# Performance work log

Measured on AMD Instinct MI355X. Metric: run time of the kernel, lower is better.

The kernel has to match this reference:

```python
import jax, jax.numpy as jnp
import numpy as np

B_, L_, H_, P_ = 8, 4096, 512, 256
DT_LO, DT_HI = 1e-3, 4e-3  # keep Heinsen log-space weights in fp32 range for L=4096


def setup_inputs() -> dict:
    key = jax.random.key(0)
    ks = jax.random.split(key, 8)
    u = jax.random.normal(ks[0], (B_, L_, H_), dtype=jnp.float32)
    # Diagonal continuous-time state matrix Lambda (HiPPO-N-like: Re=-0.5, structured imag parts)
    lambda_re = -0.5 * jnp.ones((P_,), dtype=jnp.float32)
    lambda_im = jnp.pi * (jnp.arange(P_, dtype=jnp.float32) + 1.0)
    # Input/output projections (complex, stored as re/im pairs)
    B_re = jax.random.normal(ks[1], (P_, H_), dtype=jnp.float32) / jnp.sqrt(float(H_))
    B_im = jax.random.normal(ks[2], (P_, H_), dtype=jnp.float32) / jnp.sqrt(float(H_))
    C_re = jax.random.normal(ks[3], (H_, P_), dtype=jnp.float32) / jnp.sqrt(float(P_))
    C_im = jax.random.normal(ks[4], (H_, P_), dtype=jnp.float32) / jnp.sqrt(float(P_))
    D = jax.random.normal(ks[5], (H_,), dtype=jnp.float32)
    # Per-state learnable log-timescales, log-uniform in [DT_LO, DT_HI]
    log_delta = jax.random.uniform(ks[6], (P_,), dtype=jnp.float32,
                                   minval=jnp.log(DT_LO), maxval=jnp.log(DT_HI))
    return {"u": u, "lambda_re": lambda_re, "lambda_im": lambda_im,
            "B_re": B_re, "B_im": B_im, "C_re": C_re, "C_im": C_im,
            "D": D, "log_delta": log_delta}


def reference(u, lambda_re, lambda_im, B_re, B_im, C_re, C_im, D, log_delta):
    # --- ZOH discretization (eq. 6 of S5 paper) ---
    lam = lambda_re + 1j * lambda_im                     # (P,) complex64
    delta = jnp.exp(log_delta)                           # (P,)
    lambda_bar = jnp.exp(lam * delta)                    # (P,) complex
    B_tilde = B_re + 1j * B_im                           # (P,H)
    B_bar = ((lambda_bar - 1.0) / lam)[:, None] * B_tilde  # (P,H)

    # --- input projection: Bu_k = B_bar @ u_k ---
    Bu = jnp.einsum('blh,ph->blp', u.astype(B_bar.dtype), B_bar)  # (B,L,P) complex

    # --- Heinsen log-space parallel scan: x_k = lambda_bar * x_{k-1} + Bu_k ---
    L = u.shape[1]
    log_lambda = jnp.log(lambda_bar)                     # (P,) complex
    k = jnp.arange(L, dtype=jnp.float32)
    weights = jnp.exp(k[:, None] * log_lambda[None, :])  # (L,P) complex
    xs = weights[None] * jnp.cumsum(Bu / weights[None], axis=1)  # (B,L,P)

    # --- output: y_k = 2*Re(C_tilde x_k) + D*u_k (conjugate symmetry) ---
    C_tilde = C_re + 1j * C_im                           # (H,P)
    y = 2.0 * jnp.real(jnp.einsum('blp,hp->blh', xs, C_tilde)) + D * u
    return y
```

## Files before the change

### kernel.cpp

```cpp
#include <hip/hip_runtime.h>
#include <hip/hip_bf16.h>
#include <math.h>

#define HH 512
#define PP 256
#define LSEQ 4096
#define BB 8
#define MTOT (BB*LSEQ)
#define N2P 512

typedef __attribute__((ext_vector_type(8))) short bf16x8;
typedef __attribute__((ext_vector_type(4))) float f32x4;
typedef __attribute__((ext_vector_type(8))) unsigned short u16x8;
typedef __attribute__((ext_vector_type(4))) unsigned short u16x4;

#define SWZ(row) (((((row) & 7) ^ (((row) >> 3) & 7)) << 4))

__device__ inline unsigned short f2b(float x) {
    return __builtin_bit_cast(unsigned short, __float2bfloat16(x));
}
__device__ inline float b2f(unsigned short h) {
    union { unsigned int u; float f; } v; v.u = ((unsigned int)h) << 16;
    return v.f;
}

#define GLOAD16(gp, lp) __builtin_amdgcn_global_load_lds( \
    (const __attribute__((address_space(1))) unsigned int*)(gp), \
    (__attribute__((address_space(3))) unsigned int*)(lp), 16, 0, 0)

__device__ inline size_t panel_off(int r, int k) {
    int nblk = r >> 7, rl = r & 127;
    int kblk = k >> 6, kl = k & 63;
    int c = kl >> 3, j = kl & 7;
    return (size_t)(nblk * 8 + kblk) * 16384 + rl * 128 + ((c * 16) ^ SWZ(rl)) + j * 2;
}

__global__ void prep_w1_k(const float* __restrict__ lre, const float* __restrict__ lim,
                          const float* __restrict__ logd,
                          const float* __restrict__ Bre, const float* __restrict__ Bim,
                          char* __restrict__ W1s, float2* __restrict__ lamb) {
    int idx = blockIdx.x * 256 + threadIdx.x;
    if (idx >= PP * HH) return;
    int p = idx >> 9;
    int h = idx & (HH - 1);
    float delta = expf(logd[p]);
    float lr = lre[p], li = lim[p];
    float er = expf(lr * delta);
    float th = li * delta;
    float lbr = er * cosf(th), lbi = er * sinf(th);
    if (h == 0) lamb[p] = make_float2(lbr, lbi);
    float a = lbr - 1.0f, b = lbi;
    float n2 = lr * lr + li * li;
    float gr = (a * lr + b * li) / n2;
    float gi = (b * lr - a * li) / n2;
    float br = Bre[idx], bi = Bim[idx];
    *(unsigned short*)(W1s + panel_off(p, h))      = f2b(gr * br - gi * bi);
    *(unsigned short*)(W1s + panel_off(PP + p, h)) = f2b(gr * bi + gi * br);
}

__global__ void prep_w2_k(const float* __restrict__ Cre, const float* __restrict__ Cim,
                          char* __restrict__ W2s) {
    int idx = blockIdx.x * 256 + threadIdx.x;
    if (idx >= HH * N2P) return;
    int h = idx >> 9;
    int k = idx & 511;
    float v = (k < PP) ? 2.0f * Cre[(size_t)h * PP + k]
                       : -2.0f * Cim[(size_t)h * PP + (k - PP)];
    *(unsigned short*)(W2s + panel_off(h, k)) = f2b(v);
}

#define TILE_COMPUTE(ABUF, BBUF) { \
    bf16x8 af[4][2], bfv[2][2]; \
    _Pragma("unroll") for (int f = 0; f < 4; ++f) { \
      int ar = wm + f * 16 + (lane & 15); \
      _Pragma("unroll") for (int kk = 0; kk < 2; ++kk) \
        af[f][kk] = *(const bf16x8*)((ABUF) + ar * 128 + ((kk * 64 + (lane >> 4) * 16) ^ SWZ(ar))); } \
    _Pragma("unroll") for (int g = 0; g < 2; ++g) { \
      int br = wn + g * 16 + (lane & 15); \
      _Pragma("unroll") for (int kk = 0; kk < 2; ++kk) \
        bfv[g][kk] = *(const bf16x8*)((BBUF) + br * 128 + ((kk * 64 + (lane >> 4) * 16) ^ SWZ(br))); } \
    _Pragma("unroll") for (int f = 0; f < 4; ++f) \
      _Pragma("unroll") for (int g = 0; g < 2; ++g) \
        _Pragma("unroll") for (int kk = 0; kk < 2; ++kk) \
          acc[f][g] = __builtin_amdgcn_mfma_f32_16x16x32_bf16(af[f][kk], bfv[g][kk], acc[f][g], 0, 0, 0); }

__global__ __launch_bounds__(512, 4) void gemm1_k(const float* __restrict__ u,
                                                  const char* __restrict__ W1s,
                                                  unsigned short* __restrict__ T1) {
    __shared__ char smem[65536];
    const int tid = threadIdx.x, wave = tid >> 6, lane = tid & 63;
    const int swz = (blockIdx.x & 7) * 128 + (blockIdx.x >> 3);
    const int m0 = (swz >> 2) * 128;
    const int nblk = swz & 3, n0 = nblk * 128;
    const int wm = (wave >> 2) * 64, wn = (wave & 3) * 32;
    const int arow = tid >> 2, acol = tid & 3;

    float4 av0[4], av1[4];
    f32x4 acc[4][2] = {};

#define G1_A_LOAD(SET, K0) { \
    const float* src = &u[(size_t)(m0 + arow) * HH + (K0) + acol * 16]; \
    SET[0] = *(const float4*)src;       SET[1] = *(const float4*)(src + 4); \
    SET[2] = *(const float4*)(src + 8); SET[3] = *(const float4*)(src + 12); }

#define G1_A_WRITE(SET, ABUF) { \
    bf16x8 p0, p1; \
    p0[0] = (short)f2b(SET[0].x); p0[1] = (short)f2b(SET[0].y); \
    p0[2] = (short)f2b(SET[0].z); p0[3] = (short)f2b(SET[0].w); \
    p0[4] = (short)f2b(SET[1].x); p0[5] = (short)f2b(SET[1].y); \
    p0[6] = (short)f2b(SET[1].z); p0[7] = (short)f2b(SET[1].w); \
    p1[0] = (short)f2b(SET[2].x); p1[1] = (short)f2b(SET[2].y); \
    p1[2] = (short)f2b(SET[2].z); p1[3] = (short)f2b(SET[2].w); \
    p1[4] = (short)f2b(SET[3].x); p1[5] = (short)f2b(SET[3].y); \
    p1[6] = (short)f2b(SET[3].z); p1[7] = (short)f2b(SET[3].w); \
    *(bf16x8*)((ABUF) + arow * 128 + ((acol * 32)      ^ SWZ(arow))) = p0; \
    *(bf16x8*)((ABUF) + arow * 128 + ((acol * 32 + 16) ^ SWZ(arow))) = p1; }

#define G1_B_GLOAD(K0, BBUF) { \
    const char* pan = W1s + (size_t)(nblk * 8 + ((K0) >> 6)) * 16384 + tid * 16; \
    GLOAD16(pan, (BBUF) + tid * 16); \
    GLOAD16(pan + 8192, (BBUF) + tid * 16 + 8192); }

    char* A0 = smem;          char* B0 = smem + 16384;
    char* A1 = smem + 32768;  char* B1 = smem + 49152;

    G1_A_LOAD(av1, 0);
    G1_B_GLOAD(0, B0);
    G1_A_LOAD(av0, 64);
    asm volatile("s_waitcnt vmcnt(4)" ::: "memory");
    G1_A_WRITE(av1, A0);
    __syncthreads();

    #pragma unroll
    for (int t = 0; t < 8; ++t) {
        char* Ac = (t & 1) ? A1 : A0; char* Bc = (t & 1) ? B1 : B0;
        char* An = (t & 1) ? A0 : A1; char* Bn = (t & 1) ? B0 : B1;
        if (t < 7) G1_B_GLOAD((t + 1) * 64, Bn);
        if (t < 6) {
            if ((t & 1) == 0) { G1_A_LOAD(av1, (t + 2) * 64); }
            else              { G1_A_LOAD(av0, (t + 2) * 64); }
        }
        TILE_COMPUTE(Ac, Bc);
        if (t < 7) {
            if ((t & 1) == 0) { G1_A_WRITE(av0, An); }
            else              { G1_A_WRITE(av1, An); }
        }
        if (t < 6)       { asm volatile("s_waitcnt vmcnt(4)" ::: "memory"); }
        else if (t == 6) { asm volatile("s_waitcnt vmcnt(0)" ::: "memory"); }
        __syncthreads();
    }

    {
        char* ep = smem;
        #pragma unroll
        for (int f = 0; f < 4; ++f) {
            #pragma unroll
            for (int g = 0; g < 2; ++g) {
                int r = wn + g * 16 + (lane & 15);
                int mb = (wm + f * 16 + ((lane >> 4) << 2)) * 2;
                u16x4 pk;
                pk[0] = f2b(acc[f][g][0]); pk[1] = f2b(acc[f][g][1]);
                pk[2] = f2b(acc[f][g][2]); pk[3] = f2b(acc[f][g][3]);
                *(u16x4*)(ep + r * 256 + (mb ^ ((r & 7) << 4))) = pk;
            }
        }
        __syncthreads();
        #pragma unroll
        for (int it = 0; it < 4; ++it) {
            int r = it * 32 + (tid >> 4);
            int mc = tid & 15;
            u16x8 v = *(const u16x8*)(ep + r * 256 + ((mc * 16) ^ ((r & 7) << 4)));
            *(u16x8*)&T1[(size_t)(n0 + r) * MTOT + m0 + mc * 8] = v;
        }
    }
}

__global__ __launch_bounds__(512, 4) void gemm2_k(const unsigned short* __restrict__ Xs,
                                                  const char* __restrict__ W2s,
                                                  float* __restrict__ y,
                                                  const float* __restrict__ u,
                                                  const float* __restrict__ D) {
    __shared__ char smem[65536];
    const int tid = threadIdx.x, wave = tid >> 6, lane = tid & 63;
    const int swz = (blockIdx.x & 7) * 128 + (blockIdx.x >> 3);
    const int m0 = (swz >> 2) * 128;
    const int nblk = swz & 3, n0 = nblk * 128;
    const int wm = (wave >> 2) * 64, wn = (wave & 3) * 32;
    const int kr = tid >> 5;
    const int mc4 = tid & 31;

    u16x4 xv0[4], xv1[4];
    f32x4 acc[4][2] = {};

#define G2_A_LOAD(SET, K0) { \
    _Pragma("unroll") for (int kk = 0; kk < 4; ++kk) \
        SET[kk] = *(const u16x4*)&Xs[(size_t)((K0) + kr * 4 + kk) * MTOT + m0 + mc4 * 4]; }

#define G2_A_WRITE(SET, ABUF) { \
    _Pragma("unroll") for (int j = 0; j < 4; ++j) { \
        int m = mc4 * 4 + j; \
        u16x4 o; o[0] = SET[0][j]; o[1] = SET[1][j]; o[2] = SET[2][j]; o[3] = SET[3][j]; \
        *(u16x4*)((ABUF) + m * 128 + ((kr * 8) ^ SWZ(m))) = o; } }

#define G2_B_GLOAD(K0, BBUF) { \
    const char* pan = W2s + (size_t)(nblk * 8 + ((K0) >> 6)) * 16384 + tid * 16; \
    GLOAD16(pan, (BBUF) + tid * 16); \
    GLOAD16(pan + 8192, (BBUF) + tid * 16 + 8192); }

    char* A0 = smem;          char* B0 = smem + 16384;
    char* A1 = smem + 32768;  char* B1 = smem + 49152;

    G2_A_LOAD(xv1, 0);
    G2_B_GLOAD(0, B0);
    G2_A_LOAD(xv0, 64);
    asm volatile("s_waitcnt vmcnt(4)" ::: "memory");
    G2_A_WRITE(xv1, A0);
    __syncthreads();

    #pragma unroll
    for (int t = 0; t < 8; ++t) {
        char* Ac = (t & 1) ? A1 : A0; char* Bc = (t & 1) ? B1 : B0;
        char* An = (t & 1) ? A0 : A1; char* Bn = (t & 1) ? B0 : B1;
        if (t < 7) G2_B_GLOAD((t + 1) * 64, Bn);
        if (t < 6) {
            if ((t & 1) == 0) { G2_A_LOAD(xv1, (t + 2) * 64); }
            else              { G2_A_LOAD(xv0, (t + 2) * 64); }
        }
        TILE_COMPUTE(Ac, Bc);
        if (t < 7) {
            if ((t & 1) == 0) { G2_A_WRITE(xv0, An); }
            else              { G2_A_WRITE(xv1, An); }
        }
        if (t < 6)       { asm volatile("s_waitcnt vmcnt(4)" ::: "memory"); }
        else if (t == 6) { asm volatile("s_waitcnt vmcnt(0)" ::: "memory"); }
        __syncthreads();
    }

    float* epi = (float*)smem;
    float* myepi = epi + wave * 2048;
    #pragma unroll
    for (int f = 0; f < 4; ++f) {
        #pragma unroll
        for (int g = 0; g < 2; ++g) {
            int ml = f * 16 + ((lane >> 4) << 2);
            int hl = g * 16 + (lane & 15);
            #pragma unroll
            for (int i = 0; i < 4; ++i)
                myepi[(ml + i) * 32 + hl] = acc[f][g][i];
        }
    }
    __syncthreads();

    #pragma unroll
    for (int it = 0; it < 8; ++it) {
        int idx = it * 512 + tid;
        int ml = idx >> 5, c = idx & 31;
        int w = ((ml >> 6) << 2) + (c >> 3);
        const float4 v = *(const float4*)(epi + w * 2048 + (ml & 63) * 32 + (c & 7) * 4);
        int grow = m0 + ml, gcol = n0 + c * 4;
        const float4 uv = *(const float4*)&u[(size_t)grow * HH + gcol];
        const float4 dv = *(const float4*)&D[gcol];
        float4 o = make_float4(v.x + dv.x * uv.x, v.y + dv.y * uv.y,
                               v.z + dv.z * uv.z, v.w + dv.w * uv.w);
        *(float4*)&y[(size_t)grow * HH + gcol] = o;
    }
}

__global__ __launch_bounds__(256) void scan_k(const unsigned short* __restrict__ T1,
                                              unsigned short* __restrict__ Xs,
                                              const float2* __restrict__ lamb) {
    const int b = blockIdx.x >> 8;
    const int p = blockIdx.x & 255;
    const int t = threadIdx.x;
    const float2 L = lamb[p];

    const size_t baseRe = (size_t)p * MTOT + (size_t)b * LSEQ + t * 16;
    const size_t baseIm = (size_t)(PP + p) * MTOT + (size_t)b * LSEQ + t * 16;

    u16x8 r0 = *(const u16x8*)&T1[baseRe];
    u16x8 r1 = *(const u16x8*)&T1[baseRe + 8];
    u16x8 i0 = *(const u16x8*)&T1[baseIm];
    u16x8 i1 = *(const u16x8*)&T1[baseIm + 8];

    float re[16], im[16];
    #pragma unroll
    for (int j = 0; j < 8; ++j) {
        re[j] = b2f(r0[j]); re[8 + j] = b2f(r1[j]);
        im[j] = b2f(i0[j]); im[8 + j] = b2f(i1[j]);
    }

    float sr = 0.f, si = 0.f;
    #pragma unroll
    for (int j = 0; j < 16; ++j) {
        float nsr = L.x * sr - L.y * si + re[j];
        si = L.x * si + L.y * sr + im[j];
        sr = nsr;
    }

    __shared__ float cr[256], ci[256];
    cr[t] = sr; ci[t] = si;
    __syncthreads();

    float wr = L.x, wi = L.y;
    #pragma unroll
    for (int q = 0; q < 4; ++q) { float nr = wr * wr - wi * wi; wi = 2.f * wr * wi; wr = nr; }

    for (int off = 1; off < 256; off <<= 1) {
        float pr = 0.f, pi = 0.f;
        const bool has = (t >= off);
        if (has) { pr = cr[t - off]; pi = ci[t - off]; }
        __syncthreads();
        if (has) {
            sr += wr * pr - wi * pi;
            si += wr * pi + wi * pr;
            cr[t] = sr; ci[t] = si;
        }
        __syncthreads();
        float nr = wr * wr - wi * wi; wi = 2.f * wr * wi; wr = nr;
    }

    float xr = 0.f, xi = 0.f;
    if (t > 0) { xr = cr[t - 1]; xi = ci[t - 1]; }

    u16x8 o0, o1, o2, o3;
    #pragma unroll
    for (int j = 0; j < 16; ++j) {
        float nr = L.x * xr - L.y * xi + re[j];
        xi = L.x * xi + L.y * xr + im[j];
        xr = nr;
        if (j < 8) { o0[j] = f2b(xr); o2[j] = f2b(xi); }
        else       { o1[j - 8] = f2b(xr); o3[j - 8] = f2b(xi); }
    }
    *(u16x8*)&Xs[baseRe]     = o0;
    *(u16x8*)&Xs[baseRe + 8] = o1;
    *(u16x8*)&Xs[baseIm]     = o2;
    *(u16x8*)&Xs[baseIm + 8] = o3;
}


extern "C" void kernel_launch(void* const* d_in, const int* in_sizes, int n_in,
                              void* d_out, int out_size, void* d_ws, size_t ws_size,
                              hipStream_t stream) {
    const float* u    = (const float*)d_in[0];
    const float* lre  = (const float*)d_in[1];
    const float* lim  = (const float*)d_in[2];
    const float* Bre  = (const float*)d_in[3];
    const float* Bim  = (const float*)d_in[4];
    const float* Cre  = (const float*)d_in[5];
    const float* Cim  = (const float*)d_in[6];
    const float* Dv   = (const float*)d_in[7];
    const float* logd = (const float*)d_in[8];
    float* out = (float*)d_out;

    char* ws = (char*)d_ws;
    char*           W1s  = ws;
    char*           W2s  = ws + (512 << 10);
    float2*         lamb = (float2*)(ws + (1 << 20));
    unsigned short* Xs   = (unsigned short*)(ws + (1 << 20) + 4096);

    unsigned short* T1 = (unsigned short*)d_out;

    prep_w1_k<<<(PP * HH) / 256, 256, 0, stream>>>(lre, lim, logd, Bre, Bim, W1s, lamb);
    prep_w2_k<<<(HH * N2P) / 256, 256, 0, stream>>>(Cre, Cim, W2s);

    gemm1_k<<<1024, 512, 0, stream>>>(u, W1s, T1);
    scan_k<<<BB * PP, 256, 0, stream>>>(T1, Xs, lamb);
    gemm2_k<<<1024, 512, 0, stream>>>(Xs, W2s, out, u, Dv);
}
```

Measured before the change: 97.48 us.

## Pre-convert u to swizzled bf16 panels and load GEMM1 A tiles via direct global-to-LDS copies

Adds a separate kernel that converts the fp32 input u into bf16 tiles laid out in the same swizzled panel format as the weights. GEMM1 then fetches A tiles with the same direct global-to-LDS 16-byte loads it already uses for B, instead of loading fp32 into registers, converting and writing to LDS. This removes the register staging and conversion from GEMM1 and makes the two operand pipelines uniform. The cost is an extra kernel launch and an extra pass over u: a 64 MB fp32 read plus a 32 MB bf16 write and re-read. The main loop also gains a second barrier per iteration.

```diff
diff --git a/kernel.cpp b/kernel.cpp
--- a/kernel.cpp
+++ b/kernel.cpp
@@ -69,6 +69,28 @@
     *(unsigned short*)(W2s + panel_off(h, k)) = f2b(v);
 }
 
+__global__ __launch_bounds__(256) void conv_k(const float* __restrict__ u,
+                                              char* __restrict__ ub) {
+    const int tid = threadIdx.x;
+    const int mblk = blockIdx.x >> 2;
+    const int sub = blockIdx.x & 3;
+    const int ml = sub * 32 + (tid >> 3);
+    const int kt = tid & 7;
+    const float* src = &u[(size_t)(mblk * 128 + ml) * HH + kt * 64];
+    char* dst = ub + ((size_t)(mblk * 8 + kt)) * 16384 + ml * 128;
+    #pragma unroll
+    for (int c = 0; c < 8; ++c) {
+        float4 v0 = *(const float4*)(src + c * 8);
+        float4 v1 = *(const float4*)(src + c * 8 + 4);
+        bf16x8 pk;
+        pk[0] = (short)f2b(v0.x); pk[1] = (short)f2b(v0.y);
+        pk[2] = (short)f2b(v0.z); pk[3] = (short)f2b(v0.w);
+        pk[4] = (short)f2b(v1.x); pk[5] = (short)f2b(v1.y);
+        pk[6] = (short)f2b(v1.z); pk[7] = (short)f2b(v1.w);
+        *(bf16x8*)(dst + ((c * 16) ^ SWZ(ml))) = pk;
+    }
+}
+
 #define TILE_COMPUTE(ABUF, BBUF) { \
     bf16x8 af[4][2], bfv[2][2]; \
     _Pragma("unroll") for (int f = 0; f < 4; ++f) { \
@@ -84,7 +106,7 @@
         _Pragma("unroll") for (int kk = 0; kk < 2; ++kk) \
           acc[f][g] = __builtin_amdgcn_mfma_f32_16x16x32_bf16(af[f][kk], bfv[g][kk], acc[f][g], 0, 0, 0); }
 
-__global__ __launch_bounds__(512, 4) void gemm1_k(const float* __restrict__ u,
+__global__ __launch_bounds__(512, 4) void gemm1_k(const char* __restrict__ ub,
                                                   const char* __restrict__ W1s,
                                                   unsigned short* __restrict__ T1) {
     __shared__ char smem[65536];
@@ -93,28 +115,14 @@
     const int m0 = (swz >> 2) * 128;
     const int nblk = swz & 3, n0 = nblk * 128;
     const int wm = (wave >> 2) * 64, wn = (wave & 3) * 32;
-    const int arow = tid >> 2, acol = tid & 3;
-
-    float4 av0[4], av1[4];
+    const int mblk8 = (m0 >> 7) * 8;
+
     f32x4 acc[4][2] = {};
 
-#define G1_A_LOAD(SET, K0) { \
-    const float* src = &u[(size_t)(m0 + arow) * HH + (K0) + acol * 16]; \
-    SET[0] = *(const float4*)src;       SET[1] = *(const float4*)(src + 4); \
-    SET[2] = *(const float4*)(src + 8); SET[3] = *(const float4*)(src + 12); }
-
-#define G1_A_WRITE(SET, ABUF) { \
-    bf16x8 p0, p1; \
-    p0[0] = (short)f2b(SET[0].x); p0[1] = (short)f2b(SET[0].y); \
-    p0[2] = (short)f2b(SET[0].z); p0[3] = (short)f2b(SET[0].w); \
-    p0[4] = (short)f2b(SET[1].x); p0[5] = (short)f2b(SET[1].y); \
-    p0[6] = (short)f2b(SET[1].z); p0[7] = (short)f2b(SET[1].w); \
-    p1[0] = (short)f2b(SET[2].x); p1[1] = (short)f2b(SET[2].y); \
-    p1[2] = (short)f2b(SET[2].z); p1[3] = (short)f2b(SET[2].w); \
-    p1[4] = (short)f2b(SET[3].x); p1[5] = (short)f2b(SET[3].y); \
-    p1[6] = (short)f2b(SET[3].z); p1[7] = (short)f2b(SET[3].w); \
-    *(bf16x8*)((ABUF) + arow * 128 + ((acol * 32)      ^ SWZ(arow))) = p0; \
-    *(bf16x8*)((ABUF) + arow * 128 + ((acol * 32 + 16) ^ SWZ(arow))) = p1; }
+#define G1_A_GLOAD(K0, ABUF) { \
+    const char* pan = ub + (size_t)(mblk8 + ((K0) >> 6)) * 16384 + tid * 16; \
+    GLOAD16(pan, (ABUF) + tid * 16); \
+    GLOAD16(pan + 8192, (ABUF) + tid * 16 + 8192); }
 
 #define G1_B_GLOAD(K0, BBUF) { \
     const char* pan = W1s + (size_t)(nblk * 8 + ((K0) >> 6)) * 16384 + tid * 16; \
@@ -124,29 +132,20 @@
     char* A0 = smem;          char* B0 = smem + 16384;
     char* A1 = smem + 32768;  char* B1 = smem + 49152;
 
-    G1_A_LOAD(av1, 0);
-    G1_B_GLOAD(0, B0);
-    G1_A_LOAD(av0, 64);
-    asm volatile("s_waitcnt vmcnt(4)" ::: "memory");
-    G1_A_WRITE(av1, A0);
-    __syncthreads();
+    G1_A_GLOAD(0, A0); G1_B_GLOAD(0, B0);
 
     #pragma unroll
     for (int t = 0; t < 8; ++t) {
         char* Ac = (t & 1) ? A1 : A0; char* Bc = (t & 1) ? B1 : B0;
         char* An = (t & 1) ? A0 : A1; char* Bn = (t & 1) ? B0 : B1;
-        if (t < 7) G1_B_GLOAD((t + 1) * 64, Bn);
-        if (t < 6) {
-            if ((t & 1) == 0) { G1_A_LOAD(av1, (t + 2) * 64); }
-            else              { G1_A_LOAD(av0, (t + 2) * 64); }
-        }
+        if (t < 7) {
+            G1_A_GLOAD((t + 1) * 64, An); G1_B_GLOAD((t + 1) * 64, Bn);
+            asm volatile("s_waitcnt vmcnt(4)" ::: "memory");
+        } else {
+            asm volatile("s_waitcnt vmcnt(0)" ::: "memory");
+        }
+        __syncthreads();
         TILE_COMPUTE(Ac, Bc);
-        if (t < 7) {
-            if ((t & 1) == 0) { G1_A_WRITE(av0, An); }
-            else              { G1_A_WRITE(av1, An); }
-        }
-        if (t < 6)       { asm volatile("s_waitcnt vmcnt(4)" ::: "memory"); }
-        else if (t == 6) { asm volatile("s_waitcnt vmcnt(0)" ::: "memory"); }
         __syncthreads();
     }
 
@@ -357,13 +356,15 @@
     char*           W2s  = ws + (512 << 10);
     float2*         lamb = (float2*)(ws + (1 << 20));
     unsigned short* Xs   = (unsigned short*)(ws + (1 << 20) + 4096);
+    char*           ubp  = ws + (1 << 20) + 4096 + ((size_t)32 << 20);
 
     unsigned short* T1 = (unsigned short*)d_out;
 
     prep_w1_k<<<(PP * HH) / 256, 256, 0, stream>>>(lre, lim, logd, Bre, Bim, W1s, lamb);
     prep_w2_k<<<(HH * N2P) / 256, 256, 0, stream>>>(Cre, Cim, W2s);
 
-    gemm1_k<<<1024, 512, 0, stream>>>(u, W1s, T1);
+    conv_k<<<1024, 256, 0, stream>>>(u, ubp);
+    gemm1_k<<<1024, 512, 0, stream>>>(ubp, W1s, T1);
     scan_k<<<BB * PP, 256, 0, stream>>>(T1, Xs, lamb);
     gemm2_k<<<1024, 512, 0, stream>>>(Xs, W2s, out, u, Dv);
 }
```

Measured after the change: 114.4 us. 17.3% more time.

## Process two M-tiles per gemm1 block and write outputs directly from registers

Applied to the files above, without the earlier changes.

Each gemm1 block now handles two consecutive 128-row M tiles in a single 16-step pipelined loop, so the grid is halved. The first tile's accumulators are written straight to global memory mid-loop and the pipeline keeps running into the second tile. The LDS-staged transposed epilogue is replaced by direct 8-byte stores from registers, which removes a sync and LDS traffic but gives less coalesced global writes. The aim is to amortise pipeline prologue/epilogue and overlap the first tile's stores with compute, at the cost of fewer blocks and parallelism.

```diff
diff --git a/kernel.cpp b/kernel.cpp
--- a/kernel.cpp
+++ b/kernel.cpp
@@ -89,8 +89,8 @@
                                                   unsigned short* __restrict__ T1) {
     __shared__ char smem[65536];
     const int tid = threadIdx.x, wave = tid >> 6, lane = tid & 63;
-    const int swz = (blockIdx.x & 7) * 128 + (blockIdx.x >> 3);
-    const int m0 = (swz >> 2) * 128;
+    const int swz = (blockIdx.x & 7) * 64 + (blockIdx.x >> 3);
+    const int m0 = (swz >> 2) * 256;
     const int nblk = swz & 3, n0 = nblk * 128;
     const int wm = (wave >> 2) * 64, wn = (wave & 3) * 32;
     const int arow = tid >> 2, acol = tid & 3;
@@ -98,8 +98,8 @@
     float4 av0[4], av1[4];
     f32x4 acc[4][2] = {};
 
-#define G1_A_LOAD(SET, K0) { \
-    const float* src = &u[(size_t)(m0 + arow) * HH + (K0) + acol * 16]; \
+#define G1_A_LOAD(SET, IT) { \
+    const float* src = &u[(size_t)(m0 + ((IT) >> 3) * 128 + arow) * HH + ((IT) & 7) * 64 + acol * 16]; \
     SET[0] = *(const float4*)src;       SET[1] = *(const float4*)(src + 4); \
     SET[2] = *(const float4*)(src + 8); SET[3] = *(const float4*)(src + 12); }
 
@@ -116,63 +116,60 @@
     *(bf16x8*)((ABUF) + arow * 128 + ((acol * 32)      ^ SWZ(arow))) = p0; \
     *(bf16x8*)((ABUF) + arow * 128 + ((acol * 32 + 16) ^ SWZ(arow))) = p1; }
 
-#define G1_B_GLOAD(K0, BBUF) { \
-    const char* pan = W1s + (size_t)(nblk * 8 + ((K0) >> 6)) * 16384 + tid * 16; \
+#define G1_B_GLOAD(IT, BBUF) { \
+    const char* pan = W1s + (size_t)(nblk * 8 + ((IT) & 7)) * 16384 + tid * 16; \
     GLOAD16(pan, (BBUF) + tid * 16); \
     GLOAD16(pan + 8192, (BBUF) + tid * 16 + 8192); }
 
+#define G1_C_WRITE(MT) { \
+    _Pragma("unroll") for (int f = 0; f < 4; ++f) { \
+      _Pragma("unroll") for (int g = 0; g < 2; ++g) { \
+        int r = n0 + wn + g * 16 + (lane & 15); \
+        int m = m0 + (MT) * 128 + wm + f * 16 + ((lane >> 4) << 2); \
+        u16x4 pk; \
+        pk[0] = f2b(acc[f][g][0]); pk[1] = f2b(acc[f][g][1]); \
+        pk[2] = f2b(acc[f][g][2]); pk[3] = f2b(acc[f][g][3]); \
+        *(u16x4*)&T1[(size_t)r * MTOT + m] = pk; } } }
+
     char* A0 = smem;          char* B0 = smem + 16384;
     char* A1 = smem + 32768;  char* B1 = smem + 49152;
 
     G1_A_LOAD(av1, 0);
     G1_B_GLOAD(0, B0);
-    G1_A_LOAD(av0, 64);
+    G1_A_LOAD(av0, 1);
     asm volatile("s_waitcnt vmcnt(4)" ::: "memory");
     G1_A_WRITE(av1, A0);
     __syncthreads();
 
     #pragma unroll
-    for (int t = 0; t < 8; ++t) {
-        char* Ac = (t & 1) ? A1 : A0; char* Bc = (t & 1) ? B1 : B0;
-        char* An = (t & 1) ? A0 : A1; char* Bn = (t & 1) ? B0 : B1;
-        if (t < 7) G1_B_GLOAD((t + 1) * 64, Bn);
-        if (t < 6) {
-            if ((t & 1) == 0) { G1_A_LOAD(av1, (t + 2) * 64); }
-            else              { G1_A_LOAD(av0, (t + 2) * 64); }
+    for (int it = 0; it < 16; ++it) {
+        char* Ac = (it & 1) ? A1 : A0; char* Bc = (it & 1) ? B1 : B0;
+        char* An = (it & 1) ? A0 : A1; char* Bn = (it & 1) ? B0 : B1;
+        if (it < 15) G1_B_GLOAD(it + 1, Bn);
+        if (it < 14) {
+            if ((it & 1) == 0) { G1_A_LOAD(av1, it + 2); }
+            else               { G1_A_LOAD(av0, it + 2); }
         }
         TILE_COMPUTE(Ac, Bc);
-        if (t < 7) {
-            if ((t & 1) == 0) { G1_A_WRITE(av0, An); }
-            else              { G1_A_WRITE(av1, An); }
-        }
-        if (t < 6)       { asm volatile("s_waitcnt vmcnt(4)" ::: "memory"); }
-        else if (t == 6) { asm volatile("s_waitcnt vmcnt(0)" ::: "memory"); }
-        __syncthreads();
-    }
-
-    {
-        char* ep = smem;
-        #pragma unroll
-        for (int f = 0; f < 4; ++f) {
+        if (it < 15) {
+            if ((it & 1) == 0) { G1_A_WRITE(av0, An); }
+            else               { G1_A_WRITE(av1, An); }
+        }
+        if (it == 7) {
+            G1_C_WRITE(0);
             #pragma unroll
-            for (int g = 0; g < 2; ++g) {
-                int r = wn + g * 16 + (lane & 15);
-                int mb = (wm + f * 16 + ((lane >> 4) << 2)) * 2;
-                u16x4 pk;
-                pk[0] = f2b(acc[f][g][0]); pk[1] = f2b(acc[f][g][1]);
-                pk[2] = f2b(acc[f][g][2]); pk[3] = f2b(acc[f][g][3]);
-                *(u16x4*)(ep + r * 256 + (mb ^ ((r & 7) << 4))) = pk;
-            }
-        }
-        __syncthreads();
-        #pragma unroll
-        for (int it = 0; it < 4; ++it) {
-            int r = it * 32 + (tid >> 4);
-            int mc = tid & 15;
-            u16x8 v = *(const u16x8*)(ep + r * 256 + ((mc * 16) ^ ((r & 7) << 4)));
-            *(u16x8*)&T1[(size_t)(n0 + r) * MTOT + m0 + mc * 8] = v;
-        }
-    }
+            for (int f = 0; f < 4; ++f)
+                #pragma unroll
+                for (int g = 0; g < 2; ++g) acc[f][g] = (f32x4){0.f, 0.f, 0.f, 0.f};
+            asm volatile("s_waitcnt vmcnt(12)" ::: "memory");
+        } else if (it < 14) {
+            asm volatile("s_waitcnt vmcnt(4)" ::: "memory");
+        } else if (it == 14) {
+            asm volatile("s_waitcnt vmcnt(0)" ::: "memory");
+        }
+        if (it < 15) __syncthreads();
+    }
+    G1_C_WRITE(1);
 }
 
 __global__ __launch_bounds__(512, 4) void gemm2_k(const unsigned short* __restrict__ Xs,
@@ -363,7 +360,7 @@
     prep_w1_k<<<(PP * HH) / 256, 256, 0, stream>>>(lre, lim, logd, Bre, Bim, W1s, lamb);
     prep_w2_k<<<(HH * N2P) / 256, 256, 0, stream>>>(Cre, Cim, W2s);
 
-    gemm1_k<<<1024, 512, 0, stream>>>(u, W1s, T1);
+    gemm1_k<<<512, 512, 0, stream>>>(u, W1s, T1);
     scan_k<<<BB * PP, 256, 0, stream>>>(T1, Xs, lamb);
     gemm2_k<<<1024, 512, 0, stream>>>(Xs, W2s, out, u, Dv);
 }
```

Result: slower. 102.6 us (+5.3%).
